# Kernel optimization log

Hardware: AMD Instinct MI355X
Metric: run time of the kernel (lower is better)

Reference implementation:

```python
import jax, jax.numpy as jnp
import numpy as np


def setup_inputs() -> dict:
    key = jax.random.key(0)
    k1, k2 = jax.random.split(key)
    B, F = 131072, 32
    LOCAL_DIM, RANK, UNITS = 2, 10, 8
    X = jax.random.normal(k1, (B, F), dtype=jnp.float32)
    kernel = jax.random.normal(k2, (LOCAL_DIM, RANK, F, UNITS), dtype=jnp.float32) * 0.24  # ~glorot for fan sizes here
    return {"X": X, "kernel": kernel}


def reference(X, kernel):
    # X: [B, F]; kernel: [local_dim, rank, F, units]
    local_dim = kernel.shape[0]
    # powers X^0 .. X^(local_dim-1), stacked on last axis -> [B, F, local_dim]
    powers = jnp.stack([X ** p for p in range(local_dim)], axis=-1)
    # L2-normalize over the power axis (matches tf.sqrt(reduce_sum(x**2)))
    norms = jnp.sqrt(jnp.sum(powers * powers, axis=-1, keepdims=True))
    x = powers / norms  # [B, F, local_dim]
    # per-feature matmul across all units at once: [B, F, rank, units]
    t = jnp.einsum('bfd,drfu->bfru', x, kernel)
    # hadamard product over features, then sum over CP rank -> [B, units]
    out = jnp.sum(jnp.prod(t, axis=1), axis=1)
    return out  # activation is linear (None)
```

## Files before the change

### kernel.cpp

```cpp
#include <hip/hip_runtime.h>


typedef float f32x2 __attribute__((ext_vector_type(2)));
typedef float f32x4 __attribute__((ext_vector_type(4)));

#define F 32
#define RANK 10
#define UNITS 8

__global__ __launch_bounds__(256) void cp_based_kernel(
    const float* __restrict__ X,
    const float* __restrict__ K,
    float* __restrict__ out,
    int B)
{
    const int b = blockIdx.x * blockDim.x + threadIdx.x;
    if (b >= B) return;

    const f32x4* xrow = reinterpret_cast<const f32x4*>(X + (size_t)b * F);
    float xv[F];
    float np = 1.0f;
#pragma unroll
    for (int i = 0; i < F / 4; ++i) {
        f32x4 v = xrow[i];
#pragma unroll
        for (int j = 0; j < 4; ++j) {
            float x = v[j];
            xv[i * 4 + j] = x;
            np *= __builtin_fmaf(x, x, 1.0f);
        }
    }

    const f32x4* K4 = reinterpret_cast<const f32x4*>(K);
    const int K1Q = RANK * F * UNITS / 4;

    f32x2 acc0 = {0.f, 0.f}, acc1 = {0.f, 0.f}, acc2 = {0.f, 0.f}, acc3 = {0.f, 0.f};

    for (int r = 0; r < RANK; ++r) {
        f32x2 p0 = {1.f, 1.f}, p1 = {1.f, 1.f}, p2 = {1.f, 1.f}, p3 = {1.f, 1.f};
        const int rq = r * (F * UNITS / 4);
#pragma unroll
        for (int f = 0; f < F; ++f) {
            f32x4 k0a = K4[rq + 2 * f];
            f32x4 k0b = K4[rq + 2 * f + 1];
            f32x4 k1a = K4[K1Q + rq + 2 * f];
            f32x4 k1b = K4[K1Q + rq + 2 * f + 1];
            float x = xv[f];
            f32x2 xs = {x, x};
            p0 *= xs * f32x2{k1a[0], k1a[1]} + f32x2{k0a[0], k0a[1]};
            p1 *= xs * f32x2{k1a[2], k1a[3]} + f32x2{k0a[2], k0a[3]};
            p2 *= xs * f32x2{k1b[0], k1b[1]} + f32x2{k0b[0], k0b[1]};
            p3 *= xs * f32x2{k1b[2], k1b[3]} + f32x2{k0b[2], k0b[3]};
        }
        acc0 += p0; acc1 += p1; acc2 += p2; acc3 += p3;
    }

    const float pn = __builtin_amdgcn_rsqf(np);
    acc0 *= pn; acc1 *= pn; acc2 *= pn; acc3 *= pn;

    float* o = out + (size_t)b * UNITS;
    reinterpret_cast<f32x4*>(o)[0] = f32x4{acc0[0], acc0[1], acc1[0], acc1[1]};
    reinterpret_cast<f32x4*>(o)[1] = f32x4{acc2[0], acc2[1], acc3[0], acc3[1]};
}

extern "C" void kernel_launch(void* const* d_in, const int* in_sizes, int n_in,
                              void* d_out, int out_size, void* d_ws, size_t ws_size,
                              hipStream_t stream) {
    const float* X = (const float*)d_in[0];
    const float* K = (const float*)d_in[1];
    float* out = (float*)d_out;
    const int B = in_sizes[0] / F;

    dim3 block(256);
    dim3 grid((B + 255) / 256);
    hipLaunchKernelGGL(cp_based_kernel, grid, block, 0, stream, X, K, out, B);
}
```

Measured before the change: 31.50 us.

## Map wave lanes to (rank, unit) pairs with register-resident kernel weights

Each 64-lane wave now handles 64 batch rows in sequence. Each lane owns one unit and one or two CP ranks, keeps its slice of the kernel weights in registers, and reduces across ranks with cross-lane shuffles. This replaces the old per-thread loop that reloaded every kernel weight for every batch row, cutting redundant weight loads and serial work per thread. In exchange, every lane reloads the full X row as broadcast loads, only 10 of 16 lane slots per unit do useful rank work, and the grid assumes B divides evenly by 256 with no bounds check.

```diff
diff --git a/kernel.cpp b/kernel.cpp
--- a/kernel.cpp
+++ b/kernel.cpp
@@ -2,65 +2,94 @@
 
 
 typedef float f32x2 __attribute__((ext_vector_type(2)));
-typedef float f32x4 __attribute__((ext_vector_type(4)));
 
 #define F 32
 #define RANK 10
 #define UNITS 8
+#define RPW 64
+#define WPB 4
 
-__global__ __launch_bounds__(256) void cp_based_kernel(
+__global__ __launch_bounds__(64 * WPB) void cp_based_kernel(
     const float* __restrict__ X,
     const float* __restrict__ K,
     float* __restrict__ out,
     int B)
 {
-    const int b = blockIdx.x * blockDim.x + threadIdx.x;
-    if (b >= B) return;
+    const int lane = threadIdx.x;
+    const int u = lane & 7;
+    const int s = lane >> 3;
+    const int wy = __builtin_amdgcn_readfirstlane(threadIdx.y);
+    const int wid = blockIdx.x * WPB + wy;
+    const long row0 = (long)wid * RPW;
 
-    const f32x4* xrow = reinterpret_cast<const f32x4*>(X + (size_t)b * F);
-    float xv[F];
-    float np = 1.0f;
+    f32x2 k0a[16], k1a[16], k0b[16], k1b[16];
+    {
+        const int r1 = s;
 #pragma unroll
-    for (int i = 0; i < F / 4; ++i) {
-        f32x4 v = xrow[i];
+        for (int fp = 0; fp < 16; ++fp) {
+            const int f0 = 2 * fp;
+            k0a[fp] = f32x2{K[((0 * RANK + r1) * F + f0) * UNITS + u],
+                            K[((0 * RANK + r1) * F + f0 + 1) * UNITS + u]};
+            k1a[fp] = f32x2{K[((1 * RANK + r1) * F + f0) * UNITS + u],
+                            K[((1 * RANK + r1) * F + f0 + 1) * UNITS + u]};
+        }
+    }
+    if (s < 2) {
+        const int r2 = 8 + s;
 #pragma unroll
-        for (int j = 0; j < 4; ++j) {
-            float x = v[j];
-            xv[i * 4 + j] = x;
-            np *= __builtin_fmaf(x, x, 1.0f);
+        for (int fp = 0; fp < 16; ++fp) {
+            const int f0 = 2 * fp;
+            k0b[fp] = f32x2{K[((0 * RANK + r2) * F + f0) * UNITS + u],
+                            K[((0 * RANK + r2) * F + f0 + 1) * UNITS + u]};
+            k1b[fp] = f32x2{K[((1 * RANK + r2) * F + f0) * UNITS + u],
+                            K[((1 * RANK + r2) * F + f0 + 1) * UNITS + u]};
+        }
+    } else {
+#pragma unroll
+        for (int fp = 0; fp < 16; ++fp) {
+            k0b[fp] = f32x2{0.f, 0.f};
+            k1b[fp] = f32x2{0.f, 0.f};
         }
     }
 
-    const f32x4* K4 = reinterpret_cast<const f32x4*>(K);
-    const int K1Q = RANK * F * UNITS / 4;
+    const f32x2 one2 = {1.f, 1.f};
 
-    f32x2 acc0 = {0.f, 0.f}, acc1 = {0.f, 0.f}, acc2 = {0.f, 0.f}, acc3 = {0.f, 0.f};
+#pragma unroll 2
+    for (int i = 0; i < RPW; ++i) {
+        const float* xr = X + (row0 + i) * F;
+        f32x2 xp[16];
+#pragma unroll
+        for (int fp = 0; fp < 16; ++fp)
+            xp[fp] = *reinterpret_cast<const f32x2*>(xr + 2 * fp);
 
-    for (int r = 0; r < RANK; ++r) {
-        f32x2 p0 = {1.f, 1.f}, p1 = {1.f, 1.f}, p2 = {1.f, 1.f}, p3 = {1.f, 1.f};
-        const int rq = r * (F * UNITS / 4);
+        f32x2 ta[4], tb[4], tn[4];
 #pragma unroll
-        for (int f = 0; f < F; ++f) {
-            f32x4 k0a = K4[rq + 2 * f];
-            f32x4 k0b = K4[rq + 2 * f + 1];
-            f32x4 k1a = K4[K1Q + rq + 2 * f];
-            f32x4 k1b = K4[K1Q + rq + 2 * f + 1];
-            float x = xv[f];
-            f32x2 xs = {x, x};
-            p0 *= xs * f32x2{k1a[0], k1a[1]} + f32x2{k0a[0], k0a[1]};
-            p1 *= xs * f32x2{k1a[2], k1a[3]} + f32x2{k0a[2], k0a[3]};
-            p2 *= xs * f32x2{k1b[0], k1b[1]} + f32x2{k0b[0], k0b[1]};
-            p3 *= xs * f32x2{k1b[2], k1b[3]} + f32x2{k0b[2], k0b[3]};
+        for (int q = 0; q < 4; ++q) {
+            ta[q] = xp[q] * k1a[q] + k0a[q];
+            tb[q] = xp[q] * k1b[q] + k0b[q];
+            tn[q] = xp[q] * xp[q] + one2;
         }
-        acc0 += p0; acc1 += p1; acc2 += p2; acc3 += p3;
+#pragma unroll
+        for (int fp = 4; fp < 16; ++fp) {
+            const int q = fp & 3;
+            ta[q] *= xp[fp] * k1a[fp] + k0a[fp];
+            tb[q] *= xp[fp] * k1b[fp] + k0b[fp];
+            tn[q] *= xp[fp] * xp[fp] + one2;
+        }
+        ta[0] *= ta[1]; ta[2] *= ta[3]; ta[0] *= ta[2];
+        tb[0] *= tb[1]; tb[2] *= tb[3]; tb[0] *= tb[2];
+        tn[0] *= tn[1]; tn[2] *= tn[3]; tn[0] *= tn[2];
+
+        float P = __builtin_fmaf(tb[0][0], tb[0][1], ta[0][0] * ta[0][1]);
+        float nrm = tn[0][0] * tn[0][1];
+
+        P += __shfl_xor(P, 8);
+        P += __shfl_xor(P, 16);
+        P += __shfl_xor(P, 32);
+
+        if (s == 0)
+            out[(row0 + i) * UNITS + u] = P * __builtin_amdgcn_rsqf(nrm);
     }
-
-    const float pn = __builtin_amdgcn_rsqf(np);
-    acc0 *= pn; acc1 *= pn; acc2 *= pn; acc3 *= pn;
-
-    float* o = out + (size_t)b * UNITS;
-    reinterpret_cast<f32x4*>(o)[0] = f32x4{acc0[0], acc0[1], acc1[0], acc1[1]};
-    reinterpret_cast<f32x4*>(o)[1] = f32x4{acc2[0], acc2[1], acc3[0], acc3[1]};
 }
 
 extern "C" void kernel_launch(void* const* d_in, const int* in_sizes, int n_in,
@@ -71,7 +100,7 @@
     float* out = (float*)d_out;
     const int B = in_sizes[0] / F;
 
-    dim3 block(256);
-    dim3 grid((B + 255) / 256);
+    dim3 block(64, WPB);
+    dim3 grid(B / (RPW * WPB));
     hipLaunchKernelGGL(cp_based_kernel, grid, block, 0, stream, X, K, out, B);
 }
```

New measurement: 43.77 us. +39.0%, slower.
